# Optimization experiments

Measured on AMD Instinct MI355X. Metric: run time of the kernel, lower is better.

Reference implementation:

```python
import jax, jax.numpy as jnp
import numpy as np


def setup_inputs() -> dict:
    key = jax.random.key(0)
    k1, k2 = jax.random.split(key)
    B, S, D = 64, 2048, 1024
    hidden = jax.random.normal(k1, (B, S, D), dtype=jnp.float32)
    mask = jax.random.randint(k2, (B, S), 0, 2, dtype=jnp.int32)
    return {"hidden": hidden, "mask": mask}


def reference(hidden, mask):
    # hidden: [B, S, D], mask: [B, S] (0/1)
    m = mask.astype(hidden.dtype)
    cnt = jnp.sum(m, axis=1, keepdims=True)                 # [B, 1]
    masked_sum = jnp.einsum('bsd,bs->bd', hidden, m)        # [B, D]
    masked_mean = masked_sum / jnp.clip(cnt, 1.0)           # clamp(min=1.0)
    full_mean = jnp.mean(hidden, axis=1)                    # fallback when row has no valid tokens
    return jnp.where(cnt > 0, masked_mean, full_mean)
```

## Files before the change

### kernel.cpp

```cpp
#include <hip/hip_runtime.h>

#define BB 64
#define SS 2048
#define DD 1024
#define SCHUNK 128
#define NC (SS / SCHUNK)

__global__ __launch_bounds__(256) void ep_partial(
    const float* __restrict__ hidden, const int* __restrict__ mask,
    float* __restrict__ wsm, float* __restrict__ wsf)
{
    const int b = blockIdx.x;
    const int c = blockIdx.y;
    const int s0 = c * SCHUNK;

    __shared__ float smask[SCHUNK];
    for (int i = threadIdx.x; i < SCHUNK; i += 256)
        smask[i] = (float)mask[b * SS + s0 + i];
    __syncthreads();

    const float4* hp = reinterpret_cast<const float4*>(
        hidden + ((size_t)b * SS + s0) * DD) + threadIdx.x;

    float4 am = make_float4(0.f, 0.f, 0.f, 0.f);
    float4 af = make_float4(0.f, 0.f, 0.f, 0.f);
    #pragma unroll 8
    for (int s = 0; s < SCHUNK; ++s) {
        float4 v = hp[(size_t)s * (DD / 4)];
        float  m = smask[s];
        af.x += v.x;     af.y += v.y;     af.z += v.z;     af.w += v.w;
        am.x += v.x * m; am.y += v.y * m; am.z += v.z * m; am.w += v.w * m;
    }

    const size_t o = (size_t)(b * NC + c) * (DD / 4) + threadIdx.x;
    reinterpret_cast<float4*>(wsm)[o] = am;
    reinterpret_cast<float4*>(wsf)[o] = af;
}

__global__ __launch_bounds__(256) void ep_finalize(
    const float* __restrict__ wsm, const float* __restrict__ wsf,
    const int* __restrict__ mask, float* __restrict__ out)
{
    const int b = blockIdx.x;

    __shared__ int s_cnt;
    if (threadIdx.x == 0) s_cnt = 0;
    __syncthreads();

    int local = 0;
    for (int s = threadIdx.x; s < SS; s += 256)
        local += mask[b * SS + s];
    #pragma unroll
    for (int off = 32; off > 0; off >>= 1)
        local += __shfl_down(local, off);
    if ((threadIdx.x & 63) == 0) atomicAdd(&s_cnt, local);
    __syncthreads();
    const float cnt = (float)s_cnt;

    const float4* pm = reinterpret_cast<const float4*>(wsm)
                       + (size_t)b * NC * (DD / 4) + threadIdx.x;
    const float4* pf = reinterpret_cast<const float4*>(wsf)
                       + (size_t)b * NC * (DD / 4) + threadIdx.x;

    float4 am = make_float4(0.f, 0.f, 0.f, 0.f);
    float4 af = make_float4(0.f, 0.f, 0.f, 0.f);
    #pragma unroll
    for (int c = 0; c < NC; ++c) {
        float4 vm = pm[c * (DD / 4)];
        float4 vf = pf[c * (DD / 4)];
        am.x += vm.x; am.y += vm.y; am.z += vm.z; am.w += vm.w;
        af.x += vf.x; af.y += vf.y; af.z += vf.z; af.w += vf.w;
    }

    float4 r;
    if (cnt > 0.f) {
        r.x = am.x / cnt; r.y = am.y / cnt; r.z = am.z / cnt; r.w = am.w / cnt;
    } else {
        const float invS = 1.0f / (float)SS;
        r.x = af.x * invS; r.y = af.y * invS; r.z = af.z * invS; r.w = af.w * invS;
    }
    reinterpret_cast<float4*>(out)[(size_t)b * (DD / 4) + threadIdx.x] = r;
}

extern "C" void kernel_launch(void* const* d_in, const int* in_sizes, int n_in,
                              void* d_out, int out_size, void* d_ws, size_t ws_size,
                              hipStream_t stream) {
    const float* hidden = (const float*)d_in[0];
    const int*   mask   = (const int*)d_in[1];
    float*       out    = (float*)d_out;

    float* wsm = (float*)d_ws;
    float* wsf = wsm + (size_t)BB * NC * DD;

    dim3 grid1(BB, NC);
    ep_partial<<<grid1, 256, 0, stream>>>(hidden, mask, wsm, wsf);
    ep_finalize<<<BB, 256, 0, stream>>>(wsm, wsf, mask, out);
}
```

Before: 678.7 us.

## Load only masked rows via ballot compaction; compute fallback mean lazily

The partial kernel now compacts each chunk's set mask positions into a shared index list using wave ballots and loads only those hidden rows, using nontemporal loads. This skips reading rows whose mask is zero, which for a 0/1 random mask is about half the traffic. The full-mean accumulation is dropped from the main pass and recomputed from hidden in the finalize kernel only when a row's count is zero. Per-chunk counts are written to the workspace so finalize no longer rescans the mask. The gathered rows are still contiguous 4 KB rows, so coalescing holds, but the fallback path is slow if it ever triggers.

```diff
diff --git a/kernel.cpp b/kernel.cpp
--- a/kernel.cpp
+++ b/kernel.cpp
@@ -6,80 +6,94 @@
 #define SCHUNK 128
 #define NC (SS / SCHUNK)
 
+typedef float f32x4 __attribute__((ext_vector_type(4)));
+
 __global__ __launch_bounds__(256) void ep_partial(
     const float* __restrict__ hidden, const int* __restrict__ mask,
-    float* __restrict__ wsm, float* __restrict__ wsf)
+    float* __restrict__ wsm, float* __restrict__ wscnt)
 {
-    const int b = blockIdx.x;
-    const int c = blockIdx.y;
+    const int b  = blockIdx.x;
+    const int c  = blockIdx.y;
     const int s0 = c * SCHUNK;
+    const int t  = threadIdx.x;
 
-    __shared__ float smask[SCHUNK];
-    for (int i = threadIdx.x; i < SCHUNK; i += 256)
-        smask[i] = (float)mask[b * SS + s0 + i];
+    __shared__ unsigned char sidx[SCHUNK];
+    __shared__ int s_wcnt[2];
+    __shared__ int s_n;
+
+    const int lane = t & 63;
+    const int w    = t >> 6;
+    int m = 0;
+    if (t < SCHUNK) m = (mask[b * SS + s0 + t] != 0) ? 1 : 0;
+    const unsigned long long bal = __ballot(m);
+    const int pre = __popcll(bal & ((1ull << lane) - 1ull));
+    if (t < SCHUNK && lane == 0) s_wcnt[w] = __popcll(bal);
     __syncthreads();
+    if (m) sidx[(w ? s_wcnt[0] : 0) + pre] = (unsigned char)t;
+    if (t == 0) s_n = s_wcnt[0] + s_wcnt[1];
+    __syncthreads();
+    const int n1 = s_n;
 
-    const float4* hp = reinterpret_cast<const float4*>(
-        hidden + ((size_t)b * SS + s0) * DD) + threadIdx.x;
+    const f32x4* hp = reinterpret_cast<const f32x4*>(
+        hidden + ((size_t)b * SS + s0) * DD) + t;
 
-    float4 am = make_float4(0.f, 0.f, 0.f, 0.f);
-    float4 af = make_float4(0.f, 0.f, 0.f, 0.f);
-    #pragma unroll 8
-    for (int s = 0; s < SCHUNK; ++s) {
-        float4 v = hp[(size_t)s * (DD / 4)];
-        float  m = smask[s];
-        af.x += v.x;     af.y += v.y;     af.z += v.z;     af.w += v.w;
-        am.x += v.x * m; am.y += v.y * m; am.z += v.z * m; am.w += v.w * m;
+    f32x4 am = {0.f, 0.f, 0.f, 0.f};
+
+    int i = 0;
+    for (; i + 8 <= n1; i += 8) {
+        const int i0 = sidx[i + 0], i1 = sidx[i + 1];
+        const int i2 = sidx[i + 2], i3 = sidx[i + 3];
+        const int i4 = sidx[i + 4], i5 = sidx[i + 5];
+        const int i6 = sidx[i + 6], i7 = sidx[i + 7];
+        f32x4 v0 = __builtin_nontemporal_load(hp + (size_t)i0 * (DD / 4));
+        f32x4 v1 = __builtin_nontemporal_load(hp + (size_t)i1 * (DD / 4));
+        f32x4 v2 = __builtin_nontemporal_load(hp + (size_t)i2 * (DD / 4));
+        f32x4 v3 = __builtin_nontemporal_load(hp + (size_t)i3 * (DD / 4));
+        f32x4 v4 = __builtin_nontemporal_load(hp + (size_t)i4 * (DD / 4));
+        f32x4 v5 = __builtin_nontemporal_load(hp + (size_t)i5 * (DD / 4));
+        f32x4 v6 = __builtin_nontemporal_load(hp + (size_t)i6 * (DD / 4));
+        f32x4 v7 = __builtin_nontemporal_load(hp + (size_t)i7 * (DD / 4));
+        am += v0; am += v1; am += v2; am += v3;
+        am += v4; am += v5; am += v6; am += v7;
     }
+    for (; i < n1; ++i)
+        am += __builtin_nontemporal_load(hp + (size_t)sidx[i] * (DD / 4));
 
-    const size_t o = (size_t)(b * NC + c) * (DD / 4) + threadIdx.x;
-    reinterpret_cast<float4*>(wsm)[o] = am;
-    reinterpret_cast<float4*>(wsf)[o] = af;
+    reinterpret_cast<f32x4*>(wsm)[(size_t)(b * NC + c) * (DD / 4) + t] = am;
+    if (t == 0) wscnt[b * NC + c] = (float)n1;
 }
 
-__global__ __launch_bounds__(256) void ep_finalize(
-    const float* __restrict__ wsm, const float* __restrict__ wsf,
-    const int* __restrict__ mask, float* __restrict__ out)
+__global__ __launch_bounds__(64) void ep_finalize(
+    const float* __restrict__ wsm, const float* __restrict__ wscnt,
+    const float* __restrict__ hidden, float* __restrict__ out)
 {
-    const int b = blockIdx.x;
+    const int b    = blockIdx.x;
+    const int q    = blockIdx.y;
+    const int lane = threadIdx.x;
+    const int d4   = q * 64 + lane;
 
-    __shared__ int s_cnt;
-    if (threadIdx.x == 0) s_cnt = 0;
-    __syncthreads();
+    float cnt = 0.f;
+    #pragma unroll
+    for (int c = 0; c < NC; ++c) cnt += wscnt[b * NC + c];
 
-    int local = 0;
-    for (int s = threadIdx.x; s < SS; s += 256)
-        local += mask[b * SS + s];
+    const f32x4* pm = reinterpret_cast<const f32x4*>(wsm)
+                      + (size_t)b * NC * (DD / 4) + d4;
+    f32x4 am = {0.f, 0.f, 0.f, 0.f};
     #pragma unroll
-    for (int off = 32; off > 0; off >>= 1)
-        local += __shfl_down(local, off);
-    if ((threadIdx.x & 63) == 0) atomicAdd(&s_cnt, local);
-    __syncthreads();
-    const float cnt = (float)s_cnt;
+    for (int c = 0; c < NC; ++c) am += pm[(size_t)c * (DD / 4)];
 
-    const float4* pm = reinterpret_cast<const float4*>(wsm)
-                       + (size_t)b * NC * (DD / 4) + threadIdx.x;
-    const float4* pf = reinterpret_cast<const float4*>(wsf)
-                       + (size_t)b * NC * (DD / 4) + threadIdx.x;
-
-    float4 am = make_float4(0.f, 0.f, 0.f, 0.f);
-    float4 af = make_float4(0.f, 0.f, 0.f, 0.f);
-    #pragma unroll
-    for (int c = 0; c < NC; ++c) {
-        float4 vm = pm[c * (DD / 4)];
-        float4 vf = pf[c * (DD / 4)];
-        am.x += vm.x; am.y += vm.y; am.z += vm.z; am.w += vm.w;
-        af.x += vf.x; af.y += vf.y; af.z += vf.z; af.w += vf.w;
-    }
-
-    float4 r;
+    f32x4 r;
     if (cnt > 0.f) {
         r.x = am.x / cnt; r.y = am.y / cnt; r.z = am.z / cnt; r.w = am.w / cnt;
     } else {
+        const f32x4* hp = reinterpret_cast<const f32x4*>(hidden)
+                          + (size_t)b * SS * (DD / 4) + d4;
+        f32x4 af = {0.f, 0.f, 0.f, 0.f};
+        for (int s = 0; s < SS; ++s) af += hp[(size_t)s * (DD / 4)];
         const float invS = 1.0f / (float)SS;
         r.x = af.x * invS; r.y = af.y * invS; r.z = af.z * invS; r.w = af.w * invS;
     }
-    reinterpret_cast<float4*>(out)[(size_t)b * (DD / 4) + threadIdx.x] = r;
+    reinterpret_cast<f32x4*>(out)[(size_t)b * (DD / 4) + d4] = r;
 }
 
 extern "C" void kernel_launch(void* const* d_in, const int* in_sizes, int n_in,
@@ -89,10 +103,9 @@
     const int*   mask   = (const int*)d_in[1];
     float*       out    = (float*)d_out;
 
-    float* wsm = (float*)d_ws;
-    float* wsf = wsm + (size_t)BB * NC * DD;
+    float* wsm   = (float*)d_ws;
+    float* wscnt = wsm + (size_t)BB * NC * DD;
 
-    dim3 grid1(BB, NC);
-    ep_partial<<<grid1, 256, 0, stream>>>(hidden, mask, wsm, wsf);
-    ep_finalize<<<BB, 256, 0, stream>>>(wsm, wsf, mask, out);
+    ep_partial<<<dim3(BB, NC), 256, 0, stream>>>(hidden, mask, wsm, wscnt);
+    ep_finalize<<<dim3(BB, 4), 64, 0, stream>>>(wsm, wscnt, hidden, out);
 }
```

Measured after the change: 606.4 us (median of 2 runs). -10.7%, faster.
